# Kernel optimization log

Measured on AMD Instinct MI355X. Metric: run time of the kernel, lower is better.

Reference implementation:

```python
import jax, jax.numpy as jnp
import numpy as np

B, L, V, E, H, K, T = 256, 49, 10000, 512, 512, 512, 15


def setup_inputs() -> dict:
    key = jax.random.key(0)
    ks = jax.random.split(key, 16)
    s = 0.02
    return {
        "features": jax.random.normal(ks[0], (B, L, K), dtype=jnp.float32),
        "captions": jax.random.randint(ks[1], (B, T), 0, V),
        "emb": jax.random.normal(ks[2], (V, E), dtype=jnp.float32) * s,
        "Wq": jax.random.normal(ks[3], (H, H), dtype=jnp.float32) * s,
        "bq": jnp.zeros((H,), jnp.float32),
        "Uk": jax.random.normal(ks[4], (H, K), dtype=jnp.float32) * s,
        "bk": jnp.zeros((H,), jnp.float32),
        "Va": jax.random.normal(ks[5], (1, H), dtype=jnp.float32) * s,
        "bva": jnp.zeros((1,), jnp.float32),
        "W0": jax.random.normal(ks[6], (H, K), dtype=jnp.float32) * s,
        "b0": jnp.zeros((H,), jnp.float32),
        "Wih": jax.random.normal(ks[7], (3 * H, E + H), dtype=jnp.float32) * s,
        "bih": jnp.zeros((3 * H,), jnp.float32),
        "Whh": jax.random.normal(ks[8], (3 * H, H), dtype=jnp.float32) * s,
        "bhh": jnp.zeros((3 * H,), jnp.float32),
        "W1": jax.random.normal(ks[9], (V, H), dtype=jnp.float32) * s,
        "b1": jnp.zeros((V,), jnp.float32),
    }


def reference(features, captions, emb, Wq, bq, Uk, bk, Va, bva, W0, b0, Wih, bih, Whh, bhh, W1, b1):
    # embeddings: [B, T, E]
    embeddings = emb[captions]
    # precompute key projection for additive attention: [B, L, H]
    keys_proj = jnp.einsum("blk,hk->blh", features, Uk) + bk

    def step(h, emb_t):  # h: [B,H], emb_t: [B,E]
        q = h @ Wq.T + bq                                  # [B, H]
        scores = jnp.tanh(q[:, None, :] + keys_proj) @ Va.T + bva  # [B, L, 1]
        w = jax.nn.softmax(scores, axis=1)                 # [B, L, 1]
        ctx = jnp.sum(w * features, axis=1)                # [B, K]
        ctx = ctx @ W0.T + b0                              # [B, H]
        x = jnp.concatenate([emb_t, ctx], axis=-1)         # [B, E+H]
        gi = x @ Wih.T + bih                               # [B, 3H]
        gh = h @ Whh.T + bhh                               # [B, 3H]
        i_r, i_z, i_n = jnp.split(gi, 3, axis=-1)
        h_r, h_z, h_n = jnp.split(gh, 3, axis=-1)
        r = jax.nn.sigmoid(i_r + h_r)
        z = jax.nn.sigmoid(i_z + h_z)
        n = jnp.tanh(i_n + r * h_n)
        h_new = (1.0 - z) * n + z * h
        out = h_new @ W1.T + b1                            # [B, V]
        return h_new, out

    h0 = jnp.zeros((features.shape[0], H), features.dtype)
    _, outs = jax.lax.scan(step, h0, jnp.swapaxes(embeddings, 0, 1))  # [T, B, V]
    return jnp.swapaxes(outs, 0, 1)  # [B, T, V]
```

## Files before the change

### kernel.cpp

```cpp
#include <hip/hip_runtime.h>
#include <hip/hip_bf16.h>
#include <math.h>

#define B_ 256
#define L_ 49
#define V_ 10000
#define E_ 512
#define H_ 512
#define K_ 512
#define T_ 15

typedef __bf16 bf16x8 __attribute__((ext_vector_type(8)));
typedef float f32x4 __attribute__((ext_vector_type(4)));

#define AS1 __attribute__((address_space(1)))
#define AS3 __attribute__((address_space(3)))

__device__ __forceinline__ float tanh_fast(float x)
{
    const float ax = fabsf(x);
    const float e = __expf(2.f * ax);
    const float t = 1.f - 2.f / (e + 1.f);
    return copysignf(t, x);
}

__global__ __launch_bounds__(256) void cvt_f32_bf16_kernel(
    const float* __restrict__ in, __hip_bfloat16* __restrict__ out, int n4)
{
    const int i = blockIdx.x * 256 + threadIdx.x;
    if (i >= n4) return;
    const float4 v = ((const float4*)in)[i];
    __hip_bfloat16 o[4];
    o[0] = (__hip_bfloat16)v.x; o[1] = (__hip_bfloat16)v.y;
    o[2] = (__hip_bfloat16)v.z; o[3] = (__hip_bfloat16)v.w;
    *(ushort4*)(out + (size_t)i * 4) = *(ushort4*)o;
}

__global__ __launch_bounds__(256) void transpose_cast_kernel(
    const float* __restrict__ in, __hip_bfloat16* __restrict__ out, int R, int Cc)
{
    __shared__ float tile[32][33];
    const int tr0 = blockIdx.y * 32, tc0 = blockIdx.x * 32;
    const int tx = threadIdx.x & 31, ty = threadIdx.x >> 5;
#pragma unroll
    for (int i = 0; i < 32; i += 8)
        tile[ty + i][tx] = in[(size_t)(tr0 + ty + i) * Cc + tc0 + tx];
    __syncthreads();
#pragma unroll
    for (int i = 0; i < 32; i += 8)
        out[(size_t)(tc0 + ty + i) * R + tr0 + tx] = (__hip_bfloat16)tile[tx][ty + i];
}

__global__ __launch_bounds__(256) void bfull_kernel(
    const float* __restrict__ Wih, const float* __restrict__ b0,
    const float* __restrict__ bih, float* __restrict__ bfull)
{
    const int i = blockIdx.x * 256 + threadIdx.x;
    if (i >= 3 * H_) return;
    const float* wrow = Wih + (size_t)i * (E_ + H_) + E_;
    float acc = bih[i];
    for (int j = 0; j < H_; ++j) acc += wrow[j] * b0[j];
    bfull[i] = acc;
}

__global__ __launch_bounds__(128) void emb_gather_kernel(
    const int* __restrict__ caps, const float* __restrict__ emb,
    __hip_bfloat16* __restrict__ out)
{
    const int r = blockIdx.x;
    const int t = r >> 8;
    const int b = r & 255;
    const int cap = caps[(size_t)b * T_ + t];
    const int e = threadIdx.x * 4;
    const float4 v = *(const float4*)(emb + (size_t)cap * E_ + e);
    __hip_bfloat16 o[4];
    o[0] = (__hip_bfloat16)v.x; o[1] = (__hip_bfloat16)v.y;
    o[2] = (__hip_bfloat16)v.z; o[3] = (__hip_bfloat16)v.w;
    *(ushort4*)(out + (size_t)r * E_ + e) = *(ushort4*)o;
}

template <typename OutT>
__global__ __launch_bounds__(256) void gemm_bf16_nt128_kernel(
    const __hip_bfloat16* __restrict__ A, const __hip_bfloat16* __restrict__ Bw,
    const float* __restrict__ bias, OutT* __restrict__ C,
    int N, int Kd, int lda, int ldb, int ldc, int nby)
{
    int wg = blockIdx.x;
    {
        const int nwg = gridDim.x;
        const int q = nwg >> 3, r = nwg & 7;
        const int xcd = wg & 7, idx = wg >> 3;
        wg = (xcd < r ? xcd * (q + 1) : r * (q + 1) + (xcd - r) * q) + idx;
    }
    const int by = wg % nby;
    const int bx = wg / nby;
    const int row0 = by * 128;
    const int col0 = bx * 128;

    __shared__ __hip_bfloat16 Asl[128 * 64];
    __shared__ __hip_bfloat16 Bsl[128 * 64];
    const int tid  = threadIdx.x;
    const int lane = tid & 63;
    const int w    = tid >> 6;
    const int wm   = w >> 1, wn = w & 1;

    const int srow = tid >> 3;
    const int scol = (tid & 7) << 3;

    const int lr = lane & 15;
    const int lk = (lane >> 4) << 3;

    f32x4 acc[4][4] = {};

    const __hip_bfloat16* gA = A + (size_t)(row0 + srow) * lda + scol;
    bool bv[4];
    const __hip_bfloat16* gB[4];
#pragma unroll
    for (int i = 0; i < 4; ++i) {
        const int br = col0 + i * 32 + srow;
        bv[i] = br < N;
        gB[i] = Bw + (size_t)br * ldb + scol;
    }

    for (int k0 = 0; k0 < Kd; k0 += 64) {
        __syncthreads();
#pragma unroll
        for (int i = 0; i < 4; ++i)
            __builtin_amdgcn_global_load_lds((const AS1 void*)(gA + (size_t)i * 32 * lda + k0),
                (AS3 void*)(Asl + i * 2048 + tid * 8), 16, 0, 0);
#pragma unroll
        for (int i = 0; i < 4; ++i)
            if (bv[i]) __builtin_amdgcn_global_load_lds((const AS1 void*)(gB[i] + k0),
                (AS3 void*)(Bsl + i * 2048 + tid * 8), 16, 0, 0);
        __syncthreads();

#pragma unroll
        for (int ks = 0; ks < 2; ++ks) {
            bf16x8 af[4], bfr[4];
#pragma unroll
            for (int i = 0; i < 4; ++i)
                af[i] = *(const bf16x8*)(Asl + (wm * 64 + i * 16 + lr) * 64 + ks * 32 + lk);
#pragma unroll
            for (int j = 0; j < 4; ++j)
                bfr[j] = *(const bf16x8*)(Bsl + (wn * 64 + j * 16 + lr) * 64 + ks * 32 + lk);
#pragma unroll
            for (int i = 0; i < 4; ++i)
#pragma unroll
                for (int j = 0; j < 4; ++j)
                    acc[i][j] = __builtin_amdgcn_mfma_f32_16x16x32_bf16(
                        af[i], bfr[j], acc[i][j], 0, 0, 0);
        }
    }

    const int orow = (lane >> 4) << 2;
#pragma unroll
    for (int i = 0; i < 4; ++i) {
#pragma unroll
        for (int j = 0; j < 4; ++j) {
            const int col = col0 + wn * 64 + j * 16 + lr;
            if (col >= N) continue;
            const float bvv = bias ? bias[col] : 0.f;
            const int rowb = row0 + wm * 64 + i * 16 + orow;
#pragma unroll
            for (int r = 0; r < 4; ++r)
                C[(size_t)(rowb + r) * ldc + col] = (OutT)(acc[i][j][r] + bvv);
        }
    }
}

template <typename OutT>
__device__ __forceinline__ void gemm_nt_body(
    const __hip_bfloat16* __restrict__ A, const __hip_bfloat16* __restrict__ Bw,
    const float* __restrict__ bias, const float* __restrict__ Cin, int ldcin,
    OutT* __restrict__ C, int M, int N, int Kd, int lda, int ldb, int ldc,
    int bx, int by)
{
    __shared__ __hip_bfloat16 Asl[64 * 128];
    __shared__ __hip_bfloat16 Bsl[64 * 128];
    const int tid  = threadIdx.x;
    const int lane = tid & 63;
    const int w    = tid >> 6;
    const int wm   = w >> 1, wn = w & 1;
    const int row0 = by * 64;
    const int col0 = bx * 64;

    const int srow = tid >> 4;
    const int scol = (tid & 15) << 3;

    const int lr = lane & 15;
    const int lk = (lane >> 4) << 3;

    f32x4 acc[2][2] = {};

    const __hip_bfloat16* gA = A + (size_t)(row0 + srow) * lda + scol;
    const __hip_bfloat16* gB = Bw + (size_t)(col0 + srow) * ldb + scol;

    for (int k0 = 0; k0 < Kd; k0 += 128) {
        __syncthreads();
#pragma unroll
        for (int i = 0; i < 4; ++i)
            __builtin_amdgcn_global_load_lds((const AS1 void*)(gA + (size_t)(i * 16) * lda + k0),
                (AS3 void*)(Asl + i * 2048 + tid * 8), 16, 0, 0);
#pragma unroll
        for (int i = 0; i < 4; ++i)
            __builtin_amdgcn_global_load_lds((const AS1 void*)(gB + (size_t)(i * 16) * ldb + k0),
                (AS3 void*)(Bsl + i * 2048 + tid * 8), 16, 0, 0);
        __syncthreads();

#pragma unroll
        for (int ks = 0; ks < 4; ++ks) {
            bf16x8 af[2], bfr[2];
#pragma unroll
            for (int i = 0; i < 2; ++i)
                af[i] = *(const bf16x8*)(Asl + (wm * 32 + i * 16 + lr) * 128 + ks * 32 + lk);
#pragma unroll
            for (int j = 0; j < 2; ++j)
                bfr[j] = *(const bf16x8*)(Bsl + (wn * 32 + j * 16 + lr) * 128 + ks * 32 + lk);
#pragma unroll
            for (int i = 0; i < 2; ++i)
#pragma unroll
                for (int j = 0; j < 2; ++j)
                    acc[i][j] = __builtin_amdgcn_mfma_f32_16x16x32_bf16(
                        af[i], bfr[j], acc[i][j], 0, 0, 0);
        }
    }

    const int orow = (lane >> 4) << 2;
#pragma unroll
    for (int i = 0; i < 2; ++i) {
#pragma unroll
        for (int j = 0; j < 2; ++j) {
            const int col = col0 + wn * 32 + j * 16 + lr;
            if (col >= N) continue;
            const float bvv = bias ? bias[col] : 0.f;
            const int rowb = row0 + wm * 32 + i * 16 + orow;
#pragma unroll
            for (int r = 0; r < 4; ++r) {
                float v = acc[i][j][r] + bvv;
                if (Cin) v += Cin[(size_t)(rowb + r) * ldcin + col];
                C[(size_t)(rowb + r) * ldc + col] = (OutT)v;
            }
        }
    }
}

__global__ __launch_bounds__(256) void gemm_gigh_kernel(
    const __hip_bfloat16* __restrict__ ctx, const __hip_bfloat16* __restrict__ Wf,
    const float* __restrict__ gi_emb_t,
    const __hip_bfloat16* __restrict__ hb, const __hip_bfloat16* __restrict__ Whh,
    const float* __restrict__ bhh,
    float* __restrict__ gi, float* __restrict__ gh)
{
    if (blockIdx.z == 0)
        gemm_nt_body<float>(ctx, Wf, nullptr, gi_emb_t, 3 * H_, gi,
                            B_, 3 * H_, K_, K_, K_, 3 * H_, blockIdx.x, blockIdx.y);
    else
        gemm_nt_body<float>(hb, Whh, bhh, nullptr, 0, gh,
                            B_, 3 * H_, H_, H_, H_, 3 * H_, blockIdx.x, blockIdx.y);
}

__global__ __launch_bounds__(256) void attn_gru_kernel(
    const float* __restrict__ gi, const float* __restrict__ gh,
    float* __restrict__ h, __hip_bfloat16* __restrict__ hb,
    __hip_bfloat16* __restrict__ h_all, int tprev,
    const __hip_bfloat16* __restrict__ WqT, const float* __restrict__ bq,
    const __hip_bfloat16* __restrict__ kp, const __hip_bfloat16* __restrict__ feat,
    const float* __restrict__ Va, const float* __restrict__ bva,
    __hip_bfloat16* __restrict__ ctx)
{
    const int b = blockIdx.x;
    const int tid = threadIdx.x;
    const int lane = tid & 63;
    const int wave = tid >> 6;
    __shared__ float hb_s[H_];
    __shared__ float q_part[4][H_];
    __shared__ float q_s[H_];
    __shared__ float s_sc[64];
    __shared__ float s_w[64];

    if (tprev >= 0) {
#pragma unroll
        for (int jj = 0; jj < 2; ++jj) {
            const int j = tid + jj * 256;
            const size_t o = (size_t)b * (3 * H_) + j;
            const float ir = gi[o],           hr = gh[o];
            const float iz = gi[o + H_],      hz = gh[o + H_];
            const float in_ = gi[o + 2 * H_], hn = gh[o + 2 * H_];
            const float rr = 1.f / (1.f + expf(-(ir + hr)));
            const float zz = 1.f / (1.f + expf(-(iz + hz)));
            const float nn = tanhf(in_ + rr * hn);
            const size_t hi = (size_t)b * H_ + j;
            const float hnew = (1.f - zz) * nn + zz * h[hi];
            h[hi] = hnew;
            hb_s[j] = hnew;
            const __hip_bfloat16 hv = (__hip_bfloat16)hnew;
            hb[hi] = hv;
            h_all[((size_t)b * T_ + tprev) * H_ + j] = hv;
        }
    } else {
        hb_s[tid * 2] = 0.f;
        hb_s[tid * 2 + 1] = 0.f;
    }
    __syncthreads();

    {
        const int j0 = lane * 8;
        float accq[8] = {};
        const __hip_bfloat16* wbase = WqT + (size_t)wave * 128 * H_ + j0;
#pragma unroll 4
        for (int k = 0; k < 128; ++k) {
            const float hv = hb_s[wave * 128 + k];
            const bf16x8 wv = *(const bf16x8*)(wbase + (size_t)k * H_);
#pragma unroll
            for (int i = 0; i < 8; ++i) accq[i] = fmaf(hv, (float)wv[i], accq[i]);
        }
#pragma unroll
        for (int i = 0; i < 8; ++i) q_part[wave][j0 + i] = accq[i];
    }
    __syncthreads();
    {
        const int j = tid * 2;
        q_s[j]     = bq[j]     + q_part[0][j]     + q_part[1][j]     + q_part[2][j]     + q_part[3][j];
        q_s[j + 1] = bq[j + 1] + q_part[0][j + 1] + q_part[1][j + 1] + q_part[2][j + 1] + q_part[3][j + 1];
    }
    __syncthreads();

    float qr[8], va[8];
#pragma unroll
    for (int i = 0; i < 8; ++i) {
        qr[i] = q_s[lane * 8 + i];
        va[i] = Va[lane * 8 + i];
    }

    for (int l = wave; l < L_; l += 4) {
        const bf16x8 kv = *(const bf16x8*)(kp + ((size_t)b * L_ + l) * H_ + lane * 8);
        float s = 0.f;
#pragma unroll
        for (int i = 0; i < 8; ++i) s += tanh_fast(qr[i] + (float)kv[i]) * va[i];
#pragma unroll
        for (int off = 32; off > 0; off >>= 1) s += __shfl_xor(s, off, 64);
        if (lane == 0) s_sc[l] = s + bva[0];
    }
    __syncthreads();

    if (wave == 0) {
        const float v = (lane < L_) ? s_sc[lane] : -1e30f;
        float m = v;
#pragma unroll
        for (int off = 32; off > 0; off >>= 1) m = fmaxf(m, __shfl_xor(m, off, 64));
        const float e = (lane < L_) ? expf(v - m) : 0.f;
        float ssum = e;
#pragma unroll
        for (int off = 32; off > 0; off >>= 1) ssum += __shfl_xor(ssum, off, 64);
        if (lane < L_) s_w[lane] = e / ssum;
    }
    __syncthreads();

    {
        float acc0 = 0.f, acc1 = 0.f;
        const __hip_bfloat16* fb = feat + (size_t)b * L_ * K_;
#pragma unroll 7
        for (int l = 0; l < L_; ++l) {
            const float wl = s_w[l];
            acc0 = fmaf(wl, (float)fb[(size_t)l * K_ + tid], acc0);
            acc1 = fmaf(wl, (float)fb[(size_t)l * K_ + tid + 256], acc1);
        }
        ctx[(size_t)b * K_ + tid]       = (__hip_bfloat16)acc0;
        ctx[(size_t)b * K_ + tid + 256] = (__hip_bfloat16)acc1;
    }
}

__global__ __launch_bounds__(256) void gru_kernel(
    const float* __restrict__ gi, const float* __restrict__ gh,
    float* __restrict__ h, __hip_bfloat16* __restrict__ hb,
    __hip_bfloat16* __restrict__ h_all, int t)
{
    const int idx = blockIdx.x * 256 + threadIdx.x;
    const int b = idx >> 9;
    const int j = idx & (H_ - 1);
    const size_t o = (size_t)b * 3 * H_ + j;
    const float ir = gi[o],           hr = gh[o];
    const float iz = gi[o + H_],      hz = gh[o + H_];
    const float in_ = gi[o + 2 * H_], hn = gh[o + 2 * H_];
    const float r = 1.f / (1.f + expf(-(ir + hr)));
    const float z = 1.f / (1.f + expf(-(iz + hz)));
    const float n = tanhf(in_ + r * hn);
    const float hnew = (1.f - z) * n + z * h[idx];
    h[idx] = hnew;
    const __hip_bfloat16 hv = (__hip_bfloat16)hnew;
    hb[idx] = hv;
    h_all[((size_t)b * T_ + t) * H_ + j] = hv;
}

extern "C" void kernel_launch(void* const* d_in, const int* in_sizes, int n_in,
                              void* d_out, int out_size, void* d_ws, size_t ws_size,
                              hipStream_t stream)
{
    const float* features = (const float*)d_in[0];
    const int*   captions = (const int*)d_in[1];
    const float* emb  = (const float*)d_in[2];
    const float* Wq   = (const float*)d_in[3];
    const float* bq   = (const float*)d_in[4];
    const float* Uk   = (const float*)d_in[5];
    const float* bk   = (const float*)d_in[6];
    const float* Va   = (const float*)d_in[7];
    const float* bva  = (const float*)d_in[8];
    const float* W0   = (const float*)d_in[9];
    const float* b0   = (const float*)d_in[10];
    const float* Wih  = (const float*)d_in[11];
    const float* bih  = (const float*)d_in[12];
    const float* Whh  = (const float*)d_in[13];
    const float* bhh  = (const float*)d_in[14];
    const float* W1   = (const float*)d_in[15];
    const float* b1   = (const float*)d_in[16];
    float* out = (float*)d_out;

    float* ws = (float*)d_ws;
    float* h      = ws; ws += B_ * H_;
    float* gi     = ws; ws += B_ * 3 * H_;
    float* gh     = ws; ws += B_ * 3 * H_;
    float* bfull  = ws; ws += 3 * H_;
    float* gi_emb = ws; ws += (size_t)T_ * B_ * 3 * H_;
    __hip_bfloat16* bws = (__hip_bfloat16*)ws;
    __hip_bfloat16* feat_bf = bws; bws += (size_t)B_ * L_ * K_;
    __hip_bfloat16* kp_bf   = bws; bws += (size_t)B_ * L_ * H_;
    __hip_bfloat16* W1_bf   = bws; bws += (size_t)V_ * H_;
    __hip_bfloat16* Uk_bf   = bws; bws += (size_t)H_ * K_;
    __hip_bfloat16* WqT_bf  = bws; bws += (size_t)H_ * H_;
    __hip_bfloat16* W0T_bf  = bws; bws += (size_t)K_ * H_;
    __hip_bfloat16* Wih_bf  = bws; bws += (size_t)3 * H_ * (E_ + H_);
    __hip_bfloat16* Whh_bf  = bws; bws += (size_t)3 * H_ * H_;
    __hip_bfloat16* Wfused  = bws; bws += (size_t)3 * H_ * K_;
    __hip_bfloat16* emb_all = bws; bws += (size_t)T_ * B_ * E_;
    __hip_bfloat16* hb      = bws; bws += (size_t)B_ * H_;
    __hip_bfloat16* ctx_bf  = bws; bws += (size_t)B_ * K_;
    __hip_bfloat16* h_all   = bws; bws += (size_t)B_ * T_ * H_;

    hipMemsetAsync(h, 0, (size_t)B_ * H_ * sizeof(float), stream);
    hipMemsetAsync(hb, 0, (size_t)B_ * H_ * sizeof(__hip_bfloat16), stream);

    const dim3 blk(256);
    auto cvt = [&](const float* src, __hip_bfloat16* dst, size_t n) {
        const int n4 = (int)(n / 4);
        cvt_f32_bf16_kernel<<<dim3((n4 + 255) / 256), blk, 0, stream>>>(src, dst, n4);
    };

    cvt(features, feat_bf, (size_t)B_ * L_ * K_);
    cvt(W1, W1_bf, (size_t)V_ * H_);
    cvt(Uk, Uk_bf, (size_t)H_ * K_);
    cvt(Wih, Wih_bf, (size_t)3 * H_ * (E_ + H_));
    cvt(Whh, Whh_bf, (size_t)3 * H_ * H_);
    transpose_cast_kernel<<<dim3(H_ / 32, H_ / 32), blk, 0, stream>>>(Wq, WqT_bf, H_, H_);
    transpose_cast_kernel<<<dim3(K_ / 32, H_ / 32), blk, 0, stream>>>(W0, W0T_bf, H_, K_);
    bfull_kernel<<<dim3((3 * H_ + 255) / 256), blk, 0, stream>>>(Wih, b0, bih, bfull);
    emb_gather_kernel<<<dim3(T_ * B_), dim3(128), 0, stream>>>(captions, emb, emb_all);

    gemm_bf16_nt128_kernel<__hip_bfloat16><<<dim3((B_ * L_ / 128) * (H_ / 128)), blk, 0, stream>>>(
        feat_bf, Uk_bf, bk, kp_bf, H_, K_, K_, K_, H_, B_ * L_ / 128);

    gemm_bf16_nt128_kernel<__hip_bfloat16><<<dim3((3 * H_ / 128) * (K_ / 128)), blk, 0, stream>>>(
        Wih_bf + E_, W0T_bf, nullptr, Wfused, K_, H_, E_ + H_, H_, K_, 3 * H_ / 128);

    gemm_bf16_nt128_kernel<float><<<dim3((T_ * B_ / 128) * (3 * H_ / 128)), blk, 0, stream>>>(
        emb_all, Wih_bf, bfull, gi_emb, 3 * H_, E_, E_, E_ + H_, 3 * H_, T_ * B_ / 128);

    for (int t = 0; t < T_; ++t) {
        attn_gru_kernel<<<dim3(B_), blk, 0, stream>>>(
            gi, gh, h, hb, h_all, t - 1,
            WqT_bf, bq, kp_bf, feat_bf, Va, bva, ctx_bf);
        gemm_gigh_kernel<<<dim3(3 * H_ / 64, B_ / 64, 2), blk, 0, stream>>>(
            ctx_bf, Wfused, gi_emb + (size_t)t * B_ * 3 * H_,
            hb, Whh_bf, bhh, gi, gh);
    }
    gru_kernel<<<dim3(B_ * H_ / 256), blk, 0, stream>>>(gi, gh, h, hb, h_all, T_ - 1);

    gemm_bf16_nt128_kernel<float><<<dim3((B_ * T_ / 128) * ((V_ + 127) / 128)), blk, 0, stream>>>(
        h_all, W1_bf, b1, out, V_, H_, H_, H_, V_, B_ * T_ / 128);
}
```

Before: 785.1 us.

## Double-buffer per-step GEMM, widen attention blocks, batch fp32-to-bf16 conversions

The per-step gi/gh GEMM now uses 64-wide K tiles in two LDS buffers, so the next tile's global_load_lds is issued while MFMAs run on the current one. The attention/GRU kernel moves from 256 to 512 threads per batch row, giving one element per thread and eight waves for the Wq matvec and the score loop. The five separate fp32-to-bf16 conversion launches are merged into one multi-segment kernel to cut launch overhead. The larger blocks may lower occupancy, and halving the tile size doubles the number of loop iterations and barriers.

```diff
diff --git a/kernel.cpp b/kernel.cpp
--- a/kernel.cpp
+++ b/kernel.cpp
@@ -24,16 +24,24 @@
     return copysignf(t, x);
 }
 
-__global__ __launch_bounds__(256) void cvt_f32_bf16_kernel(
-    const float* __restrict__ in, __hip_bfloat16* __restrict__ out, int n4)
-{
-    const int i = blockIdx.x * 256 + threadIdx.x;
-    if (i >= n4) return;
-    const float4 v = ((const float4*)in)[i];
+struct CvtSegs {
+    const float* src[5];
+    __hip_bfloat16* dst[5];
+    int blk_end[5];
+};
+
+__global__ __launch_bounds__(256) void cvt_multi_kernel(CvtSegs s)
+{
+    const int blk = blockIdx.x;
+    int seg = 0;
+    while (blk >= s.blk_end[seg]) ++seg;
+    const int base = seg ? s.blk_end[seg - 1] : 0;
+    const int i = (blk - base) * 256 + threadIdx.x;
+    const float4 v = ((const float4*)s.src[seg])[i];
     __hip_bfloat16 o[4];
     o[0] = (__hip_bfloat16)v.x; o[1] = (__hip_bfloat16)v.y;
     o[2] = (__hip_bfloat16)v.z; o[3] = (__hip_bfloat16)v.w;
-    *(ushort4*)(out + (size_t)i * 4) = *(ushort4*)o;
+    *(ushort4*)(s.dst[seg] + (size_t)i * 4) = *(ushort4*)o;
 }
 
 __global__ __launch_bounds__(256) void transpose_cast_kernel(
@@ -175,8 +183,8 @@
     OutT* __restrict__ C, int M, int N, int Kd, int lda, int ldb, int ldc,
     int bx, int by)
 {
-    __shared__ __hip_bfloat16 Asl[64 * 128];
-    __shared__ __hip_bfloat16 Bsl[64 * 128];
+    __shared__ __hip_bfloat16 Asl[2][64 * 64];
+    __shared__ __hip_bfloat16 Bsl[2][64 * 64];
     const int tid  = threadIdx.x;
     const int lane = tid & 63;
     const int w    = tid >> 6;
@@ -184,38 +192,47 @@
     const int row0 = by * 64;
     const int col0 = bx * 64;
 
-    const int srow = tid >> 4;
-    const int scol = (tid & 15) << 3;
+    const int srow = tid >> 3;
+    const int scol = (tid & 7) << 3;
 
     const int lr = lane & 15;
     const int lk = (lane >> 4) << 3;
 
     f32x4 acc[2][2] = {};
 
-    const __hip_bfloat16* gA = A + (size_t)(row0 + srow) * lda + scol;
-    const __hip_bfloat16* gB = Bw + (size_t)(col0 + srow) * ldb + scol;
-
-    for (int k0 = 0; k0 < Kd; k0 += 128) {
-        __syncthreads();
-#pragma unroll
-        for (int i = 0; i < 4; ++i)
-            __builtin_amdgcn_global_load_lds((const AS1 void*)(gA + (size_t)(i * 16) * lda + k0),
-                (AS3 void*)(Asl + i * 2048 + tid * 8), 16, 0, 0);
-#pragma unroll
-        for (int i = 0; i < 4; ++i)
-            __builtin_amdgcn_global_load_lds((const AS1 void*)(gB + (size_t)(i * 16) * ldb + k0),
-                (AS3 void*)(Bsl + i * 2048 + tid * 8), 16, 0, 0);
-        __syncthreads();
-
-#pragma unroll
-        for (int ks = 0; ks < 4; ++ks) {
+    const __hip_bfloat16* gA0 = A + (size_t)(row0 + srow) * lda + scol;
+    const __hip_bfloat16* gA1 = gA0 + (size_t)32 * lda;
+    const int br0 = col0 + srow, br1 = br0 + 32;
+    const __hip_bfloat16* gB0 = Bw + (size_t)br0 * ldb + scol;
+    const __hip_bfloat16* gB1 = gB0 + (size_t)32 * ldb;
+    const bool v0 = br0 < N, v1 = br1 < N;
+
+    auto stage = [&](int buf, int k0) {
+        __builtin_amdgcn_global_load_lds((const AS1 void*)(gA0 + k0),
+            (AS3 void*)(&Asl[buf][tid * 8]), 16, 0, 0);
+        __builtin_amdgcn_global_load_lds((const AS1 void*)(gA1 + k0),
+            (AS3 void*)(&Asl[buf][2048 + tid * 8]), 16, 0, 0);
+        if (v0) __builtin_amdgcn_global_load_lds((const AS1 void*)(gB0 + k0),
+            (AS3 void*)(&Bsl[buf][tid * 8]), 16, 0, 0);
+        if (v1) __builtin_amdgcn_global_load_lds((const AS1 void*)(gB1 + k0),
+            (AS3 void*)(&Bsl[buf][2048 + tid * 8]), 16, 0, 0);
+    };
+
+    stage(0, 0);
+    __syncthreads();
+    int cur = 0;
+    for (int k0 = 0; k0 < Kd; k0 += 64) {
+        if (k0 + 64 < Kd) stage(cur ^ 1, k0 + 64);
+
+#pragma unroll
+        for (int ks = 0; ks < 2; ++ks) {
             bf16x8 af[2], bfr[2];
 #pragma unroll
             for (int i = 0; i < 2; ++i)
-                af[i] = *(const bf16x8*)(Asl + (wm * 32 + i * 16 + lr) * 128 + ks * 32 + lk);
+                af[i] = *(const bf16x8*)(&Asl[cur][(wm * 32 + i * 16 + lr) * 64 + ks * 32 + lk]);
 #pragma unroll
             for (int j = 0; j < 2; ++j)
-                bfr[j] = *(const bf16x8*)(Bsl + (wn * 32 + j * 16 + lr) * 128 + ks * 32 + lk);
+                bfr[j] = *(const bf16x8*)(&Bsl[cur][(wn * 32 + j * 16 + lr) * 64 + ks * 32 + lk]);
 #pragma unroll
             for (int i = 0; i < 2; ++i)
 #pragma unroll
@@ -223,6 +240,8 @@
                     acc[i][j] = __builtin_amdgcn_mfma_f32_16x16x32_bf16(
                         af[i], bfr[j], acc[i][j], 0, 0, 0);
         }
+        __syncthreads();
+        cur ^= 1;
     }
 
     const int orow = (lane >> 4) << 2;
@@ -259,7 +278,7 @@
                             B_, 3 * H_, H_, H_, H_, 3 * H_, blockIdx.x, blockIdx.y);
 }
 
-__global__ __launch_bounds__(256) void attn_gru_kernel(
+__global__ __launch_bounds__(512) void attn_gru_kernel(
     const float* __restrict__ gi, const float* __restrict__ gh,
     float* __restrict__ h, __hip_bfloat16* __restrict__ hb,
     __hip_bfloat16* __restrict__ h_all, int tprev,
@@ -273,43 +292,39 @@
     const int lane = tid & 63;
     const int wave = tid >> 6;
     __shared__ float hb_s[H_];
-    __shared__ float q_part[4][H_];
+    __shared__ float q_part[8][H_];
     __shared__ float q_s[H_];
     __shared__ float s_sc[64];
     __shared__ float s_w[64];
 
     if (tprev >= 0) {
-#pragma unroll
-        for (int jj = 0; jj < 2; ++jj) {
-            const int j = tid + jj * 256;
-            const size_t o = (size_t)b * (3 * H_) + j;
-            const float ir = gi[o],           hr = gh[o];
-            const float iz = gi[o + H_],      hz = gh[o + H_];
-            const float in_ = gi[o + 2 * H_], hn = gh[o + 2 * H_];
-            const float rr = 1.f / (1.f + expf(-(ir + hr)));
-            const float zz = 1.f / (1.f + expf(-(iz + hz)));
-            const float nn = tanhf(in_ + rr * hn);
-            const size_t hi = (size_t)b * H_ + j;
-            const float hnew = (1.f - zz) * nn + zz * h[hi];
-            h[hi] = hnew;
-            hb_s[j] = hnew;
-            const __hip_bfloat16 hv = (__hip_bfloat16)hnew;
-            hb[hi] = hv;
-            h_all[((size_t)b * T_ + tprev) * H_ + j] = hv;
-        }
+        const int j = tid;
+        const size_t o = (size_t)b * (3 * H_) + j;
+        const float ir = gi[o],           hr = gh[o];
+        const float iz = gi[o + H_],      hz = gh[o + H_];
+        const float in_ = gi[o + 2 * H_], hn = gh[o + 2 * H_];
+        const float rr = 1.f / (1.f + expf(-(ir + hr)));
+        const float zz = 1.f / (1.f + expf(-(iz + hz)));
+        const float nn = tanhf(in_ + rr * hn);
+        const size_t hi = (size_t)b * H_ + j;
+        const float hnew = (1.f - zz) * nn + zz * h[hi];
+        h[hi] = hnew;
+        hb_s[j] = hnew;
+        const __hip_bfloat16 hv = (__hip_bfloat16)hnew;
+        hb[hi] = hv;
+        h_all[((size_t)b * T_ + tprev) * H_ + j] = hv;
     } else {
-        hb_s[tid * 2] = 0.f;
-        hb_s[tid * 2 + 1] = 0.f;
+        hb_s[tid] = 0.f;
     }
     __syncthreads();
 
     {
         const int j0 = lane * 8;
         float accq[8] = {};
-        const __hip_bfloat16* wbase = WqT + (size_t)wave * 128 * H_ + j0;
-#pragma unroll 4
-        for (int k = 0; k < 128; ++k) {
-            const float hv = hb_s[wave * 128 + k];
+        const __hip_bfloat16* wbase = WqT + (size_t)(wave * 64) * H_ + j0;
+#pragma unroll 16
+        for (int k = 0; k < 64; ++k) {
+            const float hv = hb_s[wave * 64 + k];
             const bf16x8 wv = *(const bf16x8*)(wbase + (size_t)k * H_);
 #pragma unroll
             for (int i = 0; i < 8; ++i) accq[i] = fmaf(hv, (float)wv[i], accq[i]);
@@ -319,9 +334,11 @@
     }
     __syncthreads();
     {
-        const int j = tid * 2;
-        q_s[j]     = bq[j]     + q_part[0][j]     + q_part[1][j]     + q_part[2][j]     + q_part[3][j];
-        q_s[j + 1] = bq[j + 1] + q_part[0][j + 1] + q_part[1][j + 1] + q_part[2][j + 1] + q_part[3][j + 1];
+        const int j = tid;
+        float s = bq[j];
+#pragma unroll
+        for (int w2 = 0; w2 < 8; ++w2) s += q_part[w2][j];
+        q_s[j] = s;
     }
     __syncthreads();
 
@@ -332,7 +349,7 @@
         va[i] = Va[lane * 8 + i];
     }
 
-    for (int l = wave; l < L_; l += 4) {
+    for (int l = wave; l < L_; l += 8) {
         const bf16x8 kv = *(const bf16x8*)(kp + ((size_t)b * L_ + l) * H_ + lane * 8);
         float s = 0.f;
 #pragma unroll
@@ -357,16 +374,12 @@
     __syncthreads();
 
     {
-        float acc0 = 0.f, acc1 = 0.f;
-        const __hip_bfloat16* fb = feat + (size_t)b * L_ * K_;
+        float acc0 = 0.f;
+        const __hip_bfloat16* fb = feat + (size_t)b * L_ * K_ + tid;
 #pragma unroll 7
-        for (int l = 0; l < L_; ++l) {
-            const float wl = s_w[l];
-            acc0 = fmaf(wl, (float)fb[(size_t)l * K_ + tid], acc0);
-            acc1 = fmaf(wl, (float)fb[(size_t)l * K_ + tid + 256], acc1);
-        }
-        ctx[(size_t)b * K_ + tid]       = (__hip_bfloat16)acc0;
-        ctx[(size_t)b * K_ + tid + 256] = (__hip_bfloat16)acc1;
+        for (int l = 0; l < L_; ++l)
+            acc0 = fmaf(s_w[l], (float)fb[(size_t)l * K_], acc0);
+        ctx[(size_t)b * K_ + tid] = (__hip_bfloat16)acc0;
     }
 }
 
@@ -440,16 +453,21 @@
     hipMemsetAsync(hb, 0, (size_t)B_ * H_ * sizeof(__hip_bfloat16), stream);
 
     const dim3 blk(256);
-    auto cvt = [&](const float* src, __hip_bfloat16* dst, size_t n) {
-        const int n4 = (int)(n / 4);
-        cvt_f32_bf16_kernel<<<dim3((n4 + 255) / 256), blk, 0, stream>>>(src, dst, n4);
-    };
-
-    cvt(features, feat_bf, (size_t)B_ * L_ * K_);
-    cvt(W1, W1_bf, (size_t)V_ * H_);
-    cvt(Uk, Uk_bf, (size_t)H_ * K_);
-    cvt(Wih, Wih_bf, (size_t)3 * H_ * (E_ + H_));
-    cvt(Whh, Whh_bf, (size_t)3 * H_ * H_);
+
+    {
+        CvtSegs s;
+        s.src[0] = features; s.dst[0] = feat_bf;
+        s.src[1] = W1;       s.dst[1] = W1_bf;
+        s.src[2] = Uk;       s.dst[2] = Uk_bf;
+        s.src[3] = Wih;      s.dst[3] = Wih_bf;
+        s.src[4] = Whh;      s.dst[4] = Whh_bf;
+        const int nb[5] = {
+            B_ * L_ * K_ / 1024, V_ * H_ / 1024, H_ * K_ / 1024,
+            3 * H_ * (E_ + H_) / 1024, 3 * H_ * H_ / 1024 };
+        int cum = 0;
+        for (int i = 0; i < 5; ++i) { cum += nb[i]; s.blk_end[i] = cum; }
+        cvt_multi_kernel<<<dim3(cum), blk, 0, stream>>>(s);
+    }
     transpose_cast_kernel<<<dim3(H_ / 32, H_ / 32), blk, 0, stream>>>(Wq, WqT_bf, H_, H_);
     transpose_cast_kernel<<<dim3(K_ / 32, H_ / 32), blk, 0, stream>>>(W0, W0T_bf, H_, K_);
     bfull_kernel<<<dim3((3 * H_ + 255) / 256), blk, 0, stream>>>(Wih, b0, bih, bfull);
@@ -465,7 +483,7 @@
         emb_all, Wih_bf, bfull, gi_emb, 3 * H_, E_, E_, E_ + H_, 3 * H_, T_ * B_ / 128);
 
     for (int t = 0; t < T_; ++t) {
-        attn_gru_kernel<<<dim3(B_), blk, 0, stream>>>(
+        attn_gru_kernel<<<dim3(B_), dim3(512), 0, stream>>>(
             gi, gh, h, hb, h_all, t - 1,
             WqT_bf, bq, kp_bf, feat_bf, Va, bva, ctx_bf);
         gemm_gigh_kernel<<<dim3(3 * H_ / 64, B_ / 64, 2), blk, 0, stream>>>(
```

Measured after the change: 781.4 us. No clear change (-0.5%).
